# Optimization experiments

Measured on AMD Instinct MI355X. Metric: run time of the kernel, lower is better.

The kernel has to match this reference:

```python
import jax, jax.numpy as jnp
import numpy as np

IN_SIZE = 256    # network input size
N_NODES = 1024   # hidden+output nodes, processed in topological order
DEG = 32         # fixed fan-in per node
BATCH = 16384
OUT_SIZE = 16    # last OUT_SIZE nodes are output nodes (is_output=True)


def setup_inputs() -> dict:
    key = jax.random.key(0)
    kx, kw = jax.random.split(key)
    x = jax.random.normal(kx, (BATCH, IN_SIZE), dtype=jnp.float32)
    weights = jax.random.normal(kw, (N_NODES, DEG), dtype=jnp.float32)
    # node i may only read network inputs and outputs of nodes < i
    rng = np.random.default_rng(0)
    in_idxs = np.stack([rng.integers(0, IN_SIZE + i, size=DEG) for i in range(N_NODES)])
    return {"x": x, "weights": weights, "in_idxs": jnp.asarray(in_idxs, dtype=jnp.int32)}


def reference(x, weights, in_idxs):
    B = x.shape[0]
    # activs buffer: [B, in_size + n_nodes + 1], inputs written to front
    activs = jnp.zeros((B, IN_SIZE + N_NODES + 1), dtype=x.dtype)
    activs = activs.at[:, :IN_SIZE].set(x)
    write_pos = IN_SIZE + jnp.arange(N_NODES, dtype=jnp.int32)

    def step(a, node):
        idxs, w, pos = node
        gathered = jnp.take(a, idxs, axis=1)      # [B, DEG]  index_select
        n_out = jnp.tanh(gathered @ w)            # [B]       matmul + activation
        a = a.at[:, pos].set(n_out)               # sequential write into buffer
        return a, n_out

    _, outs = jax.lax.scan(step, activs, (in_idxs, weights, write_pos))
    # output nodes are the last OUT_SIZE nodes; torch.tensor(out) stacks -> [OUT_SIZE, B]
    return outs[-OUT_SIZE:]
```

## Files before the change

kernel.cpp:

```cpp
#include <hip/hip_runtime.h>

#define IN_SIZE 256
#define N_NODES 1024
#define DEG 32
#define BATCH 16384
#define OUT_SIZE 16
#define COLS 8
#define N_ROWS (IN_SIZE + N_NODES)

__device__ __forceinline__ unsigned short f2bf_rne(float f) {
    const unsigned u = __float_as_uint(f);
    return (unsigned short)((u + 0x7FFFu + ((u >> 16) & 1u)) >> 16);
}

template <int CTRL>
__device__ __forceinline__ float dpp_add(float v) {
    return v + __int_as_float(__builtin_amdgcn_mov_dpp(__float_as_int(v), CTRL, 0xF, 0xF, true));
}

__global__ __launch_bounds__(64) void ne_detect(const void* __restrict__ xraw,
                                                int* __restrict__ flag) {
    const unsigned short* xb = (const unsigned short*)xraw;
    const int tid = threadIdx.x;
    int plausible = 0;
    for (int k = tid; k < 2048; k += 64) {
        const float v = __uint_as_float((unsigned)xb[2 * k] << 16);
        const float a = fabsf(v);
        plausible += (a == 0.0f) || (a > 1e-3f && a < 1e3f) ? 1 : 0;
    }
    for (int off = 32; off > 0; off >>= 1) plausible += __shfl_down(plausible, off);
    if (tid == 0) *flag = (plausible >= (2048 * 9) / 10) ? 1 : 0;
}

__global__ __launch_bounds__(256) void ne_prep(const void* __restrict__ wraw,
                                               const int* __restrict__ idxs,
                                               float* __restrict__ wf,
                                               float4* __restrict__ hzr,
                                               const int* __restrict__ flag) {
    const int isbf16 = *flag;
    const int tid = blockIdx.x * 256 + threadIdx.x;
    const int stride = gridDim.x * 256;
    const unsigned short* wb = (const unsigned short*)wraw;
    const float* wsrc = (const float*)wraw;
    for (int k = tid; k < N_NODES * DEG; k += stride)
        wf[k] = isbf16 ? __uint_as_float((unsigned)wb[k] << 16) : wsrc[k];
    for (int n = tid; n < N_NODES; n += stride) {
        float h1 = 0.0f, h2 = 0.0f, h3 = 0.0f;
        const int r1 = IN_SIZE + n - 1, r2 = IN_SIZE + n - 2, r3 = IN_SIZE + n - 3;
        for (int k = 0; k < DEG; ++k) {
            const int id = idxs[n * DEG + k];
            const float w = isbf16 ? __uint_as_float((unsigned)wb[n * DEG + k] << 16)
                                   : wsrc[n * DEG + k];
            if (n >= 1 && id == r1) h1 += w;
            if (n >= 2 && id == r2) h2 += w;
            if (n >= 3 && id == r3) h3 += w;
        }
        const float4 h = make_float4(h1, h2, h3, 0.0f);
#pragma unroll
        for (int r = 0; r < 8; ++r) hzr[n * 8 + r] = h;
    }
}

__global__ __launch_bounds__(64) void ne_forward(const void* __restrict__ xraw,
                                                 const float* __restrict__ wf,
                                                 const int* __restrict__ in_idxs,
                                                 const float4* __restrict__ hzr,
                                                 void* __restrict__ outraw,
                                                 const int* __restrict__ flag) {
    __shared__ float act[N_ROWS * COLS];
    const int lane = threadIdx.x;
    const int q = lane & 7;
    const int c = lane >> 3;
    const int c0 = blockIdx.x * COLS;
    const int q4 = q * 4;
    const int isbf16 = *flag;
    float* outf = (float*)outraw;
    unsigned short* outb = (unsigned short*)outraw;

    {
        float4* az = (float4*)(act + IN_SIZE * COLS);
#pragma unroll
        for (int t = 0; t < 32; ++t) az[t * 64 + lane] = make_float4(0.f, 0.f, 0.f, 0.f);
    }
    {
        const int b = c;
        if (isbf16) {
            const unsigned short* xb =
                (const unsigned short*)xraw + (size_t)(c0 + b) * IN_SIZE + q * 32;
#pragma unroll
            for (int t = 0; t < 4; ++t) {
                const uint4 v = *(const uint4*)(xb + t * 8);
                const int k0 = q * 32 + t * 8;
                act[(k0 + 0) * COLS + b] = __uint_as_float(v.x << 16);
                act[(k0 + 1) * COLS + b] = __uint_as_float(v.x & 0xFFFF0000u);
                act[(k0 + 2) * COLS + b] = __uint_as_float(v.y << 16);
                act[(k0 + 3) * COLS + b] = __uint_as_float(v.y & 0xFFFF0000u);
                act[(k0 + 4) * COLS + b] = __uint_as_float(v.z << 16);
                act[(k0 + 5) * COLS + b] = __uint_as_float(v.z & 0xFFFF0000u);
                act[(k0 + 6) * COLS + b] = __uint_as_float(v.w << 16);
                act[(k0 + 7) * COLS + b] = __uint_as_float(v.w & 0xFFFF0000u);
            }
        } else {
            const float* xs = (const float*)xraw + (size_t)(c0 + b) * IN_SIZE + q * 32;
#pragma unroll
            for (int t = 0; t < 8; ++t) {
                const float4 v = *(const float4*)(xs + t * 4);
                const int k0 = q * 32 + t * 4;
                act[(k0 + 0) * COLS + b] = v.x;
                act[(k0 + 1) * COLS + b] = v.y;
                act[(k0 + 2) * COLS + b] = v.z;
                act[(k0 + 3) * COLS + b] = v.w;
            }
        }
    }

    int4 sid[8]; float4 swt[8]; float4 shz[8];
#pragma unroll
    for (int k = 0; k < 8; ++k) {
        sid[k] = *(const int4*)(in_idxs + k * DEG + q4);
        swt[k] = *(const float4*)(wf + k * DEG + q4);
        shz[k] = hzr[k * 8 + q];
    }

    float gA0, gA1, gA2, gA3, gB0, gB1, gB2, gB3;
    { const int4 g = sid[0];
      gA0 = act[g.x * COLS + c]; gA1 = act[g.y * COLS + c];
      gA2 = act[g.z * COLS + c]; gA3 = act[g.w * COLS + c]; }
    { const int4 g = sid[1];
      gB0 = act[g.x * COLS + c]; gB1 = act[g.y * COLS + c];
      gB2 = act[g.z * COLS + c]; gB3 = act[g.w * COLS + c]; }
    float accA, accB;
    {
        const float4 wv = swt[0];
        float a = gA0 * wv.x; a = fmaf(gA1, wv.y, a);
        a = fmaf(gA2, wv.z, a); a = fmaf(gA3, wv.w, a);
        a = dpp_add<0xB1>(a); a = dpp_add<0x4E>(a); a = dpp_add<0x141>(a);
        accA = a;
    }
    { const int4 g = sid[2];
      gA0 = act[g.x * COLS + c]; gA1 = act[g.y * COLS + c];
      gA2 = act[g.z * COLS + c]; gA3 = act[g.w * COLS + c]; }

    float tp = 0.0f, tpp = 0.0f, tppp = 0.0f;

#define STEPM(i, K, S0, S1, S2, S3, ACCc, ACCn, OUT, CLAMP)                            \
    {                                                                                  \
               \
        const float4 wv = swt[((K) + 1) & 7];                                          \
        float a = S0 * wv.x; a = fmaf(S1, wv.y, a);                                    \
        a = fmaf(S2, wv.z, a); a = fmaf(S3, wv.w, a);                                  \
        a = dpp_add<0xB1>(a); a = dpp_add<0x4E>(a); a = dpp_add<0x141>(a);             \
        ACCn = a;                                                                      \
           \
        { const int4 g = sid[((K) + 3) & 7];                                           \
          S0 = act[g.x * COLS + c]; S1 = act[g.y * COLS + c];                          \
          S2 = act[g.z * COLS + c]; S3 = act[g.w * COLS + c]; }                        \
                          \
        const float4 h = shz[(K)];                                                     \
        float z = fmaf(h.z, tppp, ACCc);                                               \
        z = fmaf(h.y, tpp, z);                                                         \
        z = fmaf(h.x, tp, z);                                                          \
        const float s = __expf(-2.0f * fabsf(z));                                      \
        const float r = __builtin_amdgcn_rcpf(1.0f + s);                               \
        const float t = copysignf(fmaf(-s, r, r), z);                                  \
        if (q == 0) {                                                                  \
            act[(IN_SIZE + (i)) * COLS + c] = t;                                       \
            if (OUT) {                                                                 \
                const size_t o = (size_t)((i) - (N_NODES - OUT_SIZE)) * BATCH + c0 + c;\
                if (isbf16) outb[o] = f2bf_rne(t); else outf[o] = t;                   \
            }                                                                          \
        }                                                                              \
                    \
        { const int np = (CLAMP) ? (((i) + 8 < N_NODES) ? (i) + 8 : N_NODES - 1)       \
                                 : (i) + 8;                                            \
          sid[(K)] = *(const int4*)(in_idxs + (size_t)np * DEG + q4);                  \
          swt[(K)] = *(const float4*)(wf + (size_t)np * DEG + q4);                     \
          shz[(K)] = hzr[np * 8 + q]; }                                                \
        tppp = tpp; tpp = tp; tp = t;                                                  \
    }

#pragma unroll 1
    for (int ii = 0; ii < N_NODES - OUT_SIZE; ii += 8) {
        STEPM(ii + 0, 0, gB0, gB1, gB2, gB3, accA, accB, 0, 0)
        STEPM(ii + 1, 1, gA0, gA1, gA2, gA3, accB, accA, 0, 0)
        STEPM(ii + 2, 2, gB0, gB1, gB2, gB3, accA, accB, 0, 0)
        STEPM(ii + 3, 3, gA0, gA1, gA2, gA3, accB, accA, 0, 0)
        STEPM(ii + 4, 4, gB0, gB1, gB2, gB3, accA, accB, 0, 0)
        STEPM(ii + 5, 5, gA0, gA1, gA2, gA3, accB, accA, 0, 0)
        STEPM(ii + 6, 6, gB0, gB1, gB2, gB3, accA, accB, 0, 0)
        STEPM(ii + 7, 7, gA0, gA1, gA2, gA3, accB, accA, 0, 0)
    }
    {
        const int ii = N_NODES - OUT_SIZE;
        STEPM(ii + 0, 0, gB0, gB1, gB2, gB3, accA, accB, 1, 1)
        STEPM(ii + 1, 1, gA0, gA1, gA2, gA3, accB, accA, 1, 1)
        STEPM(ii + 2, 2, gB0, gB1, gB2, gB3, accA, accB, 1, 1)
        STEPM(ii + 3, 3, gA0, gA1, gA2, gA3, accB, accA, 1, 1)
        STEPM(ii + 4, 4, gB0, gB1, gB2, gB3, accA, accB, 1, 1)
        STEPM(ii + 5, 5, gA0, gA1, gA2, gA3, accB, accA, 1, 1)
        STEPM(ii + 6, 6, gB0, gB1, gB2, gB3, accA, accB, 1, 1)
        STEPM(ii + 7, 7, gA0, gA1, gA2, gA3, accB, accA, 1, 1)
        STEPM(ii + 8, 0, gB0, gB1, gB2, gB3, accA, accB, 1, 1)
        STEPM(ii + 9, 1, gA0, gA1, gA2, gA3, accB, accA, 1, 1)
        STEPM(ii + 10, 2, gB0, gB1, gB2, gB3, accA, accB, 1, 1)
        STEPM(ii + 11, 3, gA0, gA1, gA2, gA3, accB, accA, 1, 1)
        STEPM(ii + 12, 4, gB0, gB1, gB2, gB3, accA, accB, 1, 1)
        STEPM(ii + 13, 5, gA0, gA1, gA2, gA3, accB, accA, 1, 1)
        STEPM(ii + 14, 6, gB0, gB1, gB2, gB3, accA, accB, 1, 1)
        STEPM(ii + 15, 7, gA0, gA1, gA2, gA3, accB, accA, 1, 1)
    }
#undef STEPM
}

extern "C" void kernel_launch(void* const* d_in, const int* in_sizes, int n_in,
                              void* d_out, int out_size, void* d_ws, size_t ws_size,
                              hipStream_t stream) {
    const void* x   = d_in[0];
    const void* w   = d_in[1];
    const int* idxs = (const int*)d_in[2];

    float* wf   = (float*)d_ws;
    float4* hzr = (float4*)((char*)d_ws + (size_t)N_NODES * DEG * 4);
    int* flag   = (int*)((char*)d_ws + ((ws_size - 16) & ~(size_t)15));

    ne_detect<<<1, 64, 0, stream>>>(x, flag);
    ne_prep<<<32, 256, 0, stream>>>(w, idxs, wf, hzr, flag);

    ne_forward<<<dim3(BATCH / COLS), dim3(64), 0, stream>>>(x, wf, idxs, hzr, d_out, flag);
}
```

Baseline: 296.8 us.

## Split each node's fan-in over 16 lanes with 4 columns per block

Cuts the batch columns per 64-lane block from 8 to 4, so each column's 32-term dot product is spread over 16 lanes with 2 terms each instead of 8 lanes with 4. Indices and weights are packed into one uint4 per lane pair so a single load replaces separate index and weight loads. The goal is a shorter per-node serial chain of gathers and FMAs and twice as many blocks for latency hiding. In exchange there is one more DPP reduction step per node, and every block still walks all 1024 nodes, so total work per batch column goes up.

New measurement: 317.2 us. 6.9% more time.

```diff
diff --git a/kernel.cpp b/kernel.cpp
--- a/kernel.cpp
+++ b/kernel.cpp
@@ -5,7 +5,7 @@
 #define DEG 32
 #define BATCH 16384
 #define OUT_SIZE 16
-#define COLS 8
+#define COLS 4
 #define N_ROWS (IN_SIZE + N_NODES)
 
 __device__ __forceinline__ unsigned short f2bf_rne(float f) {
@@ -34,7 +34,7 @@
 
 __global__ __launch_bounds__(256) void ne_prep(const void* __restrict__ wraw,
                                                const int* __restrict__ idxs,
-                                               float* __restrict__ wf,
+                                               uint4* __restrict__ pk,
                                                float4* __restrict__ hzr,
                                                const int* __restrict__ flag) {
     const int isbf16 = *flag;
@@ -42,8 +42,14 @@
     const int stride = gridDim.x * 256;
     const unsigned short* wb = (const unsigned short*)wraw;
     const float* wsrc = (const float*)wraw;
-    for (int k = tid; k < N_NODES * DEG; k += stride)
-        wf[k] = isbf16 ? __uint_as_float((unsigned)wb[k] << 16) : wsrc[k];
+    for (int k = tid; k < N_NODES * 16; k += stride) {
+        const int n = k >> 4, g = k & 15;
+        const int e = n * DEG + 2 * g;
+        const float w0 = isbf16 ? __uint_as_float((unsigned)wb[e] << 16) : wsrc[e];
+        const float w1 = isbf16 ? __uint_as_float((unsigned)wb[e + 1] << 16) : wsrc[e + 1];
+        pk[k] = make_uint4((unsigned)idxs[e], (unsigned)idxs[e + 1],
+                           __float_as_uint(w0), __float_as_uint(w1));
+    }
     for (int n = tid; n < N_NODES; n += stride) {
         float h1 = 0.0f, h2 = 0.0f, h3 = 0.0f;
         const int r1 = IN_SIZE + n - 1, r2 = IN_SIZE + n - 2, r3 = IN_SIZE + n - 3;
@@ -62,17 +68,15 @@
 }
 
 __global__ __launch_bounds__(64) void ne_forward(const void* __restrict__ xraw,
-                                                 const float* __restrict__ wf,
-                                                 const int* __restrict__ in_idxs,
+                                                 const uint4* __restrict__ pk,
                                                  const float4* __restrict__ hzr,
                                                  void* __restrict__ outraw,
                                                  const int* __restrict__ flag) {
     __shared__ float act[N_ROWS * COLS];
     const int lane = threadIdx.x;
-    const int q = lane & 7;
-    const int c = lane >> 3;
+    const int q = lane & 15;
+    const int c = lane >> 4;
     const int c0 = blockIdx.x * COLS;
-    const int q4 = q * 4;
     const int isbf16 = *flag;
     float* outf = (float*)outraw;
     unsigned short* outb = (unsigned short*)outraw;
@@ -80,17 +84,17 @@
     {
         float4* az = (float4*)(act + IN_SIZE * COLS);
 #pragma unroll
-        for (int t = 0; t < 32; ++t) az[t * 64 + lane] = make_float4(0.f, 0.f, 0.f, 0.f);
+        for (int t = 0; t < 16; ++t) az[t * 64 + lane] = make_float4(0.f, 0.f, 0.f, 0.f);
     }
     {
         const int b = c;
         if (isbf16) {
             const unsigned short* xb =
-                (const unsigned short*)xraw + (size_t)(c0 + b) * IN_SIZE + q * 32;
-#pragma unroll
-            for (int t = 0; t < 4; ++t) {
+                (const unsigned short*)xraw + (size_t)(c0 + b) * IN_SIZE + q * 16;
+#pragma unroll
+            for (int t = 0; t < 2; ++t) {
                 const uint4 v = *(const uint4*)(xb + t * 8);
-                const int k0 = q * 32 + t * 8;
+                const int k0 = q * 16 + t * 8;
                 act[(k0 + 0) * COLS + b] = __uint_as_float(v.x << 16);
                 act[(k0 + 1) * COLS + b] = __uint_as_float(v.x & 0xFFFF0000u);
                 act[(k0 + 2) * COLS + b] = __uint_as_float(v.y << 16);
@@ -101,11 +105,11 @@
                 act[(k0 + 7) * COLS + b] = __uint_as_float(v.w & 0xFFFF0000u);
             }
         } else {
-            const float* xs = (const float*)xraw + (size_t)(c0 + b) * IN_SIZE + q * 32;
-#pragma unroll
-            for (int t = 0; t < 8; ++t) {
+            const float* xs = (const float*)xraw + (size_t)(c0 + b) * IN_SIZE + q * 16;
+#pragma unroll
+            for (int t = 0; t < 4; ++t) {
                 const float4 v = *(const float4*)(xs + t * 4);
-                const int k0 = q * 32 + t * 4;
+                const int k0 = q * 16 + t * 4;
                 act[(k0 + 0) * COLS + b] = v.x;
                 act[(k0 + 1) * COLS + b] = v.y;
                 act[(k0 + 2) * COLS + b] = v.z;
@@ -114,47 +118,44 @@
         }
     }
 
-    int4 sid[8]; float4 swt[8]; float4 shz[8];
+    uint4 spk[8]; float4 shz[8];
 #pragma unroll
     for (int k = 0; k < 8; ++k) {
-        sid[k] = *(const int4*)(in_idxs + k * DEG + q4);
-        swt[k] = *(const float4*)(wf + k * DEG + q4);
-        shz[k] = hzr[k * 8 + q];
-    }
-
-    float gA0, gA1, gA2, gA3, gB0, gB1, gB2, gB3;
-    { const int4 g = sid[0];
-      gA0 = act[g.x * COLS + c]; gA1 = act[g.y * COLS + c];
-      gA2 = act[g.z * COLS + c]; gA3 = act[g.w * COLS + c]; }
-    { const int4 g = sid[1];
-      gB0 = act[g.x * COLS + c]; gB1 = act[g.y * COLS + c];
-      gB2 = act[g.z * COLS + c]; gB3 = act[g.w * COLS + c]; }
+        spk[k] = pk[k * 16 + q];
+        shz[k] = hzr[k * 8 + (q & 7)];
+    }
+
+    float A0, A1, B0, B1;
+    { const uint4 g = spk[0];
+      A0 = act[(int)g.x * COLS + c]; A1 = act[(int)g.y * COLS + c]; }
+    { const uint4 g = spk[1];
+      B0 = act[(int)g.x * COLS + c]; B1 = act[(int)g.y * COLS + c]; }
     float accA, accB;
     {
-        const float4 wv = swt[0];
-        float a = gA0 * wv.x; a = fmaf(gA1, wv.y, a);
-        a = fmaf(gA2, wv.z, a); a = fmaf(gA3, wv.w, a);
-        a = dpp_add<0xB1>(a); a = dpp_add<0x4E>(a); a = dpp_add<0x141>(a);
+        const uint4 pv = spk[0];
+        float a = A0 * __uint_as_float(pv.z);
+        a = fmaf(A1, __uint_as_float(pv.w), a);
+        a = dpp_add<0x121>(a); a = dpp_add<0x122>(a);
+        a = dpp_add<0x124>(a); a = dpp_add<0x128>(a);
         accA = a;
     }
-    { const int4 g = sid[2];
-      gA0 = act[g.x * COLS + c]; gA1 = act[g.y * COLS + c];
-      gA2 = act[g.z * COLS + c]; gA3 = act[g.w * COLS + c]; }
+    { const uint4 g = spk[2];
+      A0 = act[(int)g.x * COLS + c]; A1 = act[(int)g.y * COLS + c]; }
 
     float tp = 0.0f, tpp = 0.0f, tppp = 0.0f;
 
-#define STEPM(i, K, S0, S1, S2, S3, ACCc, ACCn, OUT, CLAMP)                            \
+#define STEPM(i, K, S0, S1, ACCc, ACCn, OUT, CLAMP)                                    \
     {                                                                                  \
-               \
-        const float4 wv = swt[((K) + 1) & 7];                                          \
-        float a = S0 * wv.x; a = fmaf(S1, wv.y, a);                                    \
-        a = fmaf(S2, wv.z, a); a = fmaf(S3, wv.w, a);                                  \
-        a = dpp_add<0xB1>(a); a = dpp_add<0x4E>(a); a = dpp_add<0x141>(a);             \
+                       \
+        const uint4 pv = spk[((K) + 1) & 7];                                           \
+        float a = S0 * __uint_as_float(pv.z);                                          \
+        a = fmaf(S1, __uint_as_float(pv.w), a);                                        \
+        a = dpp_add<0x121>(a); a = dpp_add<0x122>(a);                                  \
+        a = dpp_add<0x124>(a); a = dpp_add<0x128>(a);                                  \
         ACCn = a;                                                                      \
            \
-        { const int4 g = sid[((K) + 3) & 7];                                           \
-          S0 = act[g.x * COLS + c]; S1 = act[g.y * COLS + c];                          \
-          S2 = act[g.z * COLS + c]; S3 = act[g.w * COLS + c]; }                        \
+        { const uint4 g = spk[((K) + 3) & 7];                                          \
+          S0 = act[(int)g.x * COLS + c]; S1 = act[(int)g.y * COLS + c]; }              \
                           \
         const float4 h = shz[(K)];                                                     \
         float z = fmaf(h.z, tppp, ACCc);                                               \
@@ -170,44 +171,43 @@
                 if (isbf16) outb[o] = f2bf_rne(t); else outf[o] = t;                   \
             }                                                                          \
         }                                                                              \
-                    \
+                      \
         { const int np = (CLAMP) ? (((i) + 8 < N_NODES) ? (i) + 8 : N_NODES - 1)       \
                                  : (i) + 8;                                            \
-          sid[(K)] = *(const int4*)(in_idxs + (size_t)np * DEG + q4);                  \
-          swt[(K)] = *(const float4*)(wf + (size_t)np * DEG + q4);                     \
-          shz[(K)] = hzr[np * 8 + q]; }                                                \
+          spk[(K)] = pk[np * 16 + q];                                                  \
+          shz[(K)] = hzr[np * 8 + (q & 7)]; }                                          \
         tppp = tpp; tpp = tp; tp = t;                                                  \
     }
 
 #pragma unroll 1
     for (int ii = 0; ii < N_NODES - OUT_SIZE; ii += 8) {
-        STEPM(ii + 0, 0, gB0, gB1, gB2, gB3, accA, accB, 0, 0)
-        STEPM(ii + 1, 1, gA0, gA1, gA2, gA3, accB, accA, 0, 0)
-        STEPM(ii + 2, 2, gB0, gB1, gB2, gB3, accA, accB, 0, 0)
-        STEPM(ii + 3, 3, gA0, gA1, gA2, gA3, accB, accA, 0, 0)
-        STEPM(ii + 4, 4, gB0, gB1, gB2, gB3, accA, accB, 0, 0)
-        STEPM(ii + 5, 5, gA0, gA1, gA2, gA3, accB, accA, 0, 0)
-        STEPM(ii + 6, 6, gB0, gB1, gB2, gB3, accA, accB, 0, 0)
-        STEPM(ii + 7, 7, gA0, gA1, gA2, gA3, accB, accA, 0, 0)
+        STEPM(ii + 0, 0, B0, B1, accA, accB, 0, 0)
+        STEPM(ii + 1, 1, A0, A1, accB, accA, 0, 0)
+        STEPM(ii + 2, 2, B0, B1, accA, accB, 0, 0)
+        STEPM(ii + 3, 3, A0, A1, accB, accA, 0, 0)
+        STEPM(ii + 4, 4, B0, B1, accA, accB, 0, 0)
+        STEPM(ii + 5, 5, A0, A1, accB, accA, 0, 0)
+        STEPM(ii + 6, 6, B0, B1, accA, accB, 0, 0)
+        STEPM(ii + 7, 7, A0, A1, accB, accA, 0, 0)
     }
     {
         const int ii = N_NODES - OUT_SIZE;
-        STEPM(ii + 0, 0, gB0, gB1, gB2, gB3, accA, accB, 1, 1)
-        STEPM(ii + 1, 1, gA0, gA1, gA2, gA3, accB, accA, 1, 1)
-        STEPM(ii + 2, 2, gB0, gB1, gB2, gB3, accA, accB, 1, 1)
-        STEPM(ii + 3, 3, gA0, gA1, gA2, gA3, accB, accA, 1, 1)
-        STEPM(ii + 4, 4, gB0, gB1, gB2, gB3, accA, accB, 1, 1)
-        STEPM(ii + 5, 5, gA0, gA1, gA2, gA3, accB, accA, 1, 1)
-        STEPM(ii + 6, 6, gB0, gB1, gB2, gB3, accA, accB, 1, 1)
-        STEPM(ii + 7, 7, gA0, gA1, gA2, gA3, accB, accA, 1, 1)
-        STEPM(ii + 8, 0, gB0, gB1, gB2, gB3, accA, accB, 1, 1)
-        STEPM(ii + 9, 1, gA0, gA1, gA2, gA3, accB, accA, 1, 1)
-        STEPM(ii + 10, 2, gB0, gB1, gB2, gB3, accA, accB, 1, 1)
-        STEPM(ii + 11, 3, gA0, gA1, gA2, gA3, accB, accA, 1, 1)
-        STEPM(ii + 12, 4, gB0, gB1, gB2, gB3, accA, accB, 1, 1)
-        STEPM(ii + 13, 5, gA0, gA1, gA2, gA3, accB, accA, 1, 1)
-        STEPM(ii + 14, 6, gB0, gB1, gB2, gB3, accA, accB, 1, 1)
-        STEPM(ii + 15, 7, gA0, gA1, gA2, gA3, accB, accA, 1, 1)
+        STEPM(ii + 0, 0, B0, B1, accA, accB, 1, 1)
+        STEPM(ii + 1, 1, A0, A1, accB, accA, 1, 1)
+        STEPM(ii + 2, 2, B0, B1, accA, accB, 1, 1)
+        STEPM(ii + 3, 3, A0, A1, accB, accA, 1, 1)
+        STEPM(ii + 4, 4, B0, B1, accA, accB, 1, 1)
+        STEPM(ii + 5, 5, A0, A1, accB, accA, 1, 1)
+        STEPM(ii + 6, 6, B0, B1, accA, accB, 1, 1)
+        STEPM(ii + 7, 7, A0, A1, accB, accA, 1, 1)
+        STEPM(ii + 8, 0, B0, B1, accA, accB, 1, 1)
+        STEPM(ii + 9, 1, A0, A1, accB, accA, 1, 1)
+        STEPM(ii + 10, 2, B0, B1, accA, accB, 1, 1)
+        STEPM(ii + 11, 3, A0, A1, accB, accA, 1, 1)
+        STEPM(ii + 12, 4, B0, B1, accA, accB, 1, 1)
+        STEPM(ii + 13, 5, A0, A1, accB, accA, 1, 1)
+        STEPM(ii + 14, 6, B0, B1, accA, accB, 1, 1)
+        STEPM(ii + 15, 7, A0, A1, accB, accA, 1, 1)
     }
 #undef STEPM
 }
@@ -219,12 +219,12 @@
     const void* w   = d_in[1];
     const int* idxs = (const int*)d_in[2];
 
-    float* wf   = (float*)d_ws;
-    float4* hzr = (float4*)((char*)d_ws + (size_t)N_NODES * DEG * 4);
+    uint4* pk   = (uint4*)d_ws;
+    float4* hzr = (float4*)((char*)d_ws + (size_t)N_NODES * 16 * 16);
     int* flag   = (int*)((char*)d_ws + ((ws_size - 16) & ~(size_t)15));
 
     ne_detect<<<1, 64, 0, stream>>>(x, flag);
-    ne_prep<<<32, 256, 0, stream>>>(w, idxs, wf, hzr, flag);
-
-    ne_forward<<<dim3(BATCH / COLS), dim3(64), 0, stream>>>(x, wf, idxs, hzr, d_out, flag);
-}
+    ne_prep<<<32, 256, 0, stream>>>(w, idxs, pk, hzr, flag);
+
+    ne_forward<<<dim3(BATCH / COLS), dim3(64), 0, stream>>>(x, pk, hzr, d_out, flag);
+}
```
